# Optimization experiments

Hardware: AMD Instinct MI355X
Metric: run time of the kernel (lower is better)

The kernel has to match this reference:

```python
import jax, jax.numpy as jnp
import numpy as np

EMBED_DIM = 1024
NUM_HEADS = 16
HEAD_DIM = EMBED_DIM // NUM_HEADS


def setup_inputs() -> dict:
    key = jax.random.key(0)
    k_x, k_qkv, k_out = jax.random.split(key, 3)
    x = jax.random.normal(k_x, (4, 2048, EMBED_DIM), dtype=jnp.float32)
    # torch Linear weight [out, in]; y = x @ W.T
    scale = 1.0 / np.sqrt(EMBED_DIM)
    W_qkv = jax.random.uniform(k_qkv, (3 * EMBED_DIM, EMBED_DIM), dtype=jnp.float32, minval=-scale, maxval=scale)
    W_out = jax.random.uniform(k_out, (EMBED_DIM, EMBED_DIM), dtype=jnp.float32, minval=-scale, maxval=scale)
    return {"x": x, "W_qkv": W_qkv, "W_out": W_out}


def reference(x, W_qkv, W_out):
    B, S, E = x.shape
    qkv = jnp.einsum('bse,fe->bsf', x, W_qkv)                     # [B,S,3E]
    qkv = qkv.reshape(B, S, 3, NUM_HEADS, HEAD_DIM)
    qkv = jnp.transpose(qkv, (2, 0, 3, 1, 4))                     # [3,B,H,S,D]
    q, k, v = qkv[0], qkv[1], qkv[2]
    scores = jnp.einsum('bhqd,bhkd->bhqk', q, k) / np.sqrt(HEAD_DIM)
    attn = jax.nn.softmax(scores, axis=-1)                        # dropout_p=0 (eval)
    out = jnp.einsum('bhqk,bhkd->bhqd', attn, v)                  # [B,H,S,D]
    out = jnp.transpose(out, (0, 2, 1, 3)).reshape(B, S, E)
    return jnp.einsum('bse,fe->bsf', out, W_out)
```

## Files before the change

kernel.cpp:

```cpp
#include <hip/hip_runtime.h>
#include <hip/hip_bf16.h>
#include <stdint.h>

#define DEVI __device__ __forceinline__

typedef float  f32x4 __attribute__((ext_vector_type(4)));
typedef short  s16x8 __attribute__((ext_vector_type(8)));

DEVI unsigned short bfbits(float f) {
  __hip_bfloat16 h = __float2bfloat16(f);
  return __builtin_bit_cast(unsigned short, h);
}

DEVI void mfma_bf16(f32x4& d, s16x8 a, s16x8 b) {
  asm("v_mfma_f32_16x16x32_bf16 %0, %1, %2, %0" : "+v"(d) : "v"(a), "v"(b));
}

DEVI void gload_lds16(const void* g, void* l) {
  __builtin_amdgcn_global_load_lds(
      (const __attribute__((address_space(1))) void*)g,
      (__attribute__((address_space(3))) void*)l, 16, 0, 0);
}

__global__ void cvtk(const float4* __restrict__ src, ushort4* __restrict__ dst, int n4) {
  int i = blockIdx.x * blockDim.x + threadIdx.x;
  int st = gridDim.x * blockDim.x;
  for (; i < n4; i += st) {
    float4 v = src[i];
    ushort4 o;
    o.x = bfbits(v.x); o.y = bfbits(v.y); o.z = bfbits(v.z); o.w = bfbits(v.w);
    dst[i] = o;
  }
}

template<int EPI>
__global__ __launch_bounds__(256) void gemm_k(
    const unsigned short* __restrict__ A,
    const unsigned short* __restrict__ BT,
    unsigned short* __restrict__ q_ws,
    unsigned short* __restrict__ k_ws,
    unsigned short* __restrict__ vt_ws,
    float* __restrict__ Cout)
{
  constexpr int K = 1024;
  __shared__ __align__(16) unsigned short Als[128 * 64];
  __shared__ __align__(16) unsigned short Bls[128 * 64];

  const int tid = threadIdx.x;
  const int w = tid >> 6, l = tid & 63;
  const int g = l >> 4, c = l & 15;
  const int wm = w >> 1, wn = w & 1;
  const int nb = blockIdx.x, mb = blockIdx.y;

  int srow[4], skof[4];
#pragma unroll
  for (int it = 0; it < 4; ++it) {
    int idx = (w * 4 + it) * 64 + l;
    srow[it] = idx >> 3;
    skof[it] = ((idx & 7) ^ (srow[it] & 7)) << 3;
  }

  f32x4 acc[4][4] = {};
  const unsigned short* Ab = A + (size_t)(mb * 128) * K;
  const unsigned short* Bb = BT + (size_t)(nb * 128) * K;

  for (int kt = 0; kt < K / 64; ++kt) {
    __syncthreads();
#pragma unroll
    for (int it = 0; it < 4; ++it) {
      gload_lds16(Ab + (size_t)srow[it] * K + kt * 64 + skof[it], &Als[(w * 4 + it) * 512]);
      gload_lds16(Bb + (size_t)srow[it] * K + kt * 64 + skof[it], &Bls[(w * 4 + it) * 512]);
    }
    __syncthreads();
#pragma unroll
    for (int kk = 0; kk < 2; ++kk) {
      s16x8 af[4], bfv[4];
#pragma unroll
      for (int mi = 0; mi < 4; ++mi) {
        int row = wm * 64 + mi * 16 + c;
        int slot = (kk * 4 + g) ^ (row & 7);
        af[mi] = *(const s16x8*)&Als[row * 64 + slot * 8];
      }
#pragma unroll
      for (int ni = 0; ni < 4; ++ni) {
        int row = wn * 64 + ni * 16 + c;
        int slot = (kk * 4 + g) ^ (row & 7);
        bfv[ni] = *(const s16x8*)&Bls[row * 64 + slot * 8];
      }
#pragma unroll
      for (int mi = 0; mi < 4; ++mi)
#pragma unroll
        for (int ni = 0; ni < 4; ++ni)
          mfma_bf16(acc[mi][ni], af[mi], bfv[ni]);
    }
  }

  if constexpr (EPI == 0) {
    const int csec = (nb * 128) >> 10;
#pragma unroll
    for (int mi = 0; mi < 4; ++mi) {
#pragma unroll
      for (int ni = 0; ni < 4; ++ni) {
        int ncol = nb * 128 + wn * 64 + ni * 16 + c;
        int f = ncol & 1023;
        int hh = f >> 6, dd = f & 63;
#pragma unroll
        for (int r = 0; r < 4; ++r) {
          int m = mb * 128 + wm * 64 + mi * 16 + 4 * g + r;
          int bb = m >> 11, ss = m & 2047;
          int bh = bb * 16 + hh;
          float v = acc[mi][ni][r];
          if (csec == 0)      q_ws[((size_t)bh * 2048 + ss) * 64 + dd] = bfbits(v * 0.125f);
          else if (csec == 1) k_ws[((size_t)bh * 2048 + ss) * 64 + dd] = bfbits(v);
          else                vt_ws[((size_t)bh * 64 + dd) * 2048 + ss] = bfbits(v);
        }
      }
    }
  } else {
#pragma unroll
    for (int mi = 0; mi < 4; ++mi)
#pragma unroll
      for (int ni = 0; ni < 4; ++ni) {
        int ncol = nb * 128 + wn * 64 + ni * 16 + c;
#pragma unroll
        for (int r = 0; r < 4; ++r) {
          int m = mb * 128 + wm * 64 + mi * 16 + 4 * g + r;
          Cout[(size_t)m * 1024 + ncol] = acc[mi][ni][r];
        }
      }
  }
}

__global__ __launch_bounds__(256) void attn_k(
    const unsigned short* __restrict__ q_ws,
    const unsigned short* __restrict__ k_ws,
    const unsigned short* __restrict__ vt_ws,
    unsigned short* __restrict__ a_ws)
{
  __shared__ __align__(16) unsigned short P[4][64][40];
  const int tid = threadIdx.x;
  const int w = tid >> 6, l = tid & 63;
  const int g = l >> 4, c = l & 15;
  const int wid = blockIdx.x * 4 + w;
  const int bh = wid >> 5, qt = wid & 31;
  const int b = bh >> 4, h = bh & 15;
  const int qbase = qt * 64;

  const unsigned short* qp = q_ws + (size_t)bh * 2048 * 64;
  const unsigned short* kp = k_ws + (size_t)bh * 2048 * 64;
  const unsigned short* vp = vt_ws + (size_t)bh * 64 * 2048;

  s16x8 qa[4][2];
#pragma unroll
  for (int mi = 0; mi < 4; ++mi)
#pragma unroll
    for (int kk = 0; kk < 2; ++kk)
      qa[mi][kk] = *(const s16x8*)&qp[(size_t)(qbase + mi * 16 + c) * 64 + kk * 32 + g * 8];

  f32x4 o[4][4] = {};
  float lrun[4];
#pragma unroll
  for (int mi = 0; mi < 4; ++mi) lrun[mi] = 0.f;

  s16x8 kb[2][2], vb[4];
#pragma unroll
  for (int nt = 0; nt < 2; ++nt)
#pragma unroll
    for (int kk = 0; kk < 2; ++kk)
      kb[nt][kk] = *(const s16x8*)&kp[(size_t)(nt * 16 + c) * 64 + kk * 32 + g * 8];
#pragma unroll
  for (int dt = 0; dt < 4; ++dt)
    vb[dt] = *(const s16x8*)&vp[(size_t)(dt * 16 + c) * 2048 + g * 8];

  for (int kv = 0; kv < 2048; kv += 32) {
    const int nkv = (kv + 32 < 2048) ? kv + 32 : kv;
    s16x8 kbn[2][2], vbn[4];
#pragma unroll
    for (int nt = 0; nt < 2; ++nt)
#pragma unroll
      for (int kk = 0; kk < 2; ++kk)
        kbn[nt][kk] = *(const s16x8*)&kp[(size_t)(nkv + nt * 16 + c) * 64 + kk * 32 + g * 8];
#pragma unroll
    for (int dt = 0; dt < 4; ++dt)
      vbn[dt] = *(const s16x8*)&vp[(size_t)(dt * 16 + c) * 2048 + nkv + g * 8];

    f32x4 st[4][2] = {};
#pragma unroll
    for (int kk = 0; kk < 2; ++kk)
#pragma unroll
      for (int mi = 0; mi < 4; ++mi)
#pragma unroll
        for (int nt = 0; nt < 2; ++nt)
          mfma_bf16(st[mi][nt], kb[nt][kk], qa[mi][kk]);

#pragma unroll
    for (int mi = 0; mi < 4; ++mi) {
      f32x4 s0 = st[mi][0], s1 = st[mi][1];
      ushort4 w0, w1;
      float p00 = __expf(s0[0]), p01 = __expf(s0[1]);
      float p02 = __expf(s0[2]), p03 = __expf(s0[3]);
      float p10 = __expf(s1[0]), p11 = __expf(s1[1]);
      float p12 = __expf(s1[2]), p13 = __expf(s1[3]);
      lrun[mi] += ((p00 + p01) + (p02 + p03)) + ((p10 + p11) + (p12 + p13));
      w0.x = bfbits(p00); w0.y = bfbits(p01); w0.z = bfbits(p02); w0.w = bfbits(p03);
      w1.x = bfbits(p10); w1.y = bfbits(p11); w1.z = bfbits(p12); w1.w = bfbits(p13);
      *(ushort4*)&P[w][mi * 16 + c][4 * g]      = w0;
      *(ushort4*)&P[w][mi * 16 + c][16 + 4 * g] = w1;
    }

    asm volatile("s_waitcnt lgkmcnt(0)" ::: "memory");
    __builtin_amdgcn_sched_barrier(0);

    s16x8 pa[4];
#pragma unroll
    for (int mi = 0; mi < 4; ++mi)
      pa[mi] = *(const s16x8*)&P[w][mi * 16 + c][g * 8];

    __builtin_amdgcn_sched_barrier(0);
    asm volatile("" ::: "memory");

#pragma unroll
    for (int dt = 0; dt < 4; ++dt)
#pragma unroll
      for (int mi = 0; mi < 4; ++mi)
        mfma_bf16(o[dt][mi], vb[dt], pa[mi]);

#pragma unroll
    for (int nt = 0; nt < 2; ++nt)
#pragma unroll
      for (int kk = 0; kk < 2; ++kk)
        kb[nt][kk] = kbn[nt][kk];
#pragma unroll
    for (int dt = 0; dt < 4; ++dt)
      vb[dt] = vbn[dt];
  }

#pragma unroll
  for (int mi = 0; mi < 4; ++mi) {
    float lv = lrun[mi];
    lv += __shfl_xor(lv, 16);
    lv += __shfl_xor(lv, 32);
    float inv = 1.0f / lv;
    size_t base = ((size_t)(b * 2048 + qbase + mi * 16 + c)) * 1024 + h * 64;
#pragma unroll
    for (int dt = 0; dt < 4; ++dt) {
      ushort4 ov;
      ov.x = bfbits(o[dt][mi][0] * inv);
      ov.y = bfbits(o[dt][mi][1] * inv);
      ov.z = bfbits(o[dt][mi][2] * inv);
      ov.w = bfbits(o[dt][mi][3] * inv);
      *(ushort4*)&a_ws[base + dt * 16 + 4 * g] = ov;
    }
  }
}

extern "C" void kernel_launch(void* const* d_in, const int* in_sizes, int n_in,
                              void* d_out, int out_size, void* d_ws, size_t ws_size,
                              hipStream_t stream) {
  const float* x    = (const float*)d_in[0];
  const float* Wqkv = (const float*)d_in[1];
  const float* Wout = (const float*)d_in[2];

  unsigned short* xb    = (unsigned short*)d_ws;
  unsigned short* wqkvb = xb    + (size_t)8192 * 1024;
  unsigned short* woutb = wqkvb + (size_t)3072 * 1024;
  unsigned short* q_ws  = woutb + (size_t)1024 * 1024;
  unsigned short* k_ws  = q_ws  + (size_t)64 * 2048 * 64;
  unsigned short* vt_ws = k_ws  + (size_t)64 * 2048 * 64;
  unsigned short* a_ws  = xb;

  cvtk<<<1024, 256, 0, stream>>>((const float4*)x,    (ushort4*)xb,    8192 * 1024 / 4);
  cvtk<<<512,  256, 0, stream>>>((const float4*)Wqkv, (ushort4*)wqkvb, 3072 * 1024 / 4);
  cvtk<<<256,  256, 0, stream>>>((const float4*)Wout, (ushort4*)woutb, 1024 * 1024 / 4);

  gemm_k<0><<<dim3(24, 64), 256, 0, stream>>>(xb, wqkvb, q_ws, k_ws, vt_ws, nullptr);
  attn_k<<<512, 256, 0, stream>>>(q_ws, k_ws, vt_ws, a_ws);
  gemm_k<1><<<dim3(8, 64), 256, 0, stream>>>(a_ws, woutb, nullptr, nullptr, nullptr, (float*)d_out);
}
```

Measured before the change: 250.9 us.

## Split attention KV range in two and merge partial outputs

The attention kernel is templated so each query tile processes only half of the key/value sequence. This doubles the grid from 512 to 1024 blocks to fill more of the GPU. Each half writes an unnormalized bf16 partial output and its row sums, and a new merge kernel adds the halves and normalizes. The cost is an extra kernel launch, extra workspace traffic for the partials, and an extra bf16 rounding of the partial outputs. The split path only runs when the workspace is large enough; otherwise the original single-pass path is used.

```diff
diff --git a/kernel.cpp b/kernel.cpp
--- a/kernel.cpp
+++ b/kernel.cpp
@@ -10,6 +10,10 @@
 DEVI unsigned short bfbits(float f) {
   __hip_bfloat16 h = __float2bfloat16(f);
   return __builtin_bit_cast(unsigned short, h);
+}
+DEVI float b2f(unsigned short u) {
+  unsigned int x = ((unsigned int)u) << 16;
+  return __builtin_bit_cast(float, x);
 }
 
 DEVI void mfma_bf16(f32x4& d, s16x8 a, s16x8 b) {
@@ -131,24 +135,32 @@
   }
 }
 
+template<int SPLIT>
 __global__ __launch_bounds__(256) void attn_k(
     const unsigned short* __restrict__ q_ws,
     const unsigned short* __restrict__ k_ws,
     const unsigned short* __restrict__ vt_ws,
-    unsigned short* __restrict__ a_ws)
+    unsigned short* __restrict__ a_ws,
+    unsigned short* __restrict__ opA,
+    unsigned short* __restrict__ opB,
+    float* __restrict__ lA,
+    float* __restrict__ lB)
 {
   __shared__ __align__(16) unsigned short P[4][64][40];
   const int tid = threadIdx.x;
   const int w = tid >> 6, l = tid & 63;
   const int g = l >> 4, c = l & 15;
-  const int wid = blockIdx.x * 4 + w;
+  const int kvh  = SPLIT ? (blockIdx.x >> 9) : 0;
+  const int bidq = SPLIT ? (blockIdx.x & 511) : blockIdx.x;
+  const int wid = bidq * 4 + w;
   const int bh = wid >> 5, qt = wid & 31;
   const int b = bh >> 4, h = bh & 15;
   const int qbase = qt * 64;
+  const int KVLEN = SPLIT ? 1024 : 2048;
 
   const unsigned short* qp = q_ws + (size_t)bh * 2048 * 64;
-  const unsigned short* kp = k_ws + (size_t)bh * 2048 * 64;
-  const unsigned short* vp = vt_ws + (size_t)bh * 64 * 2048;
+  const unsigned short* kp = k_ws + (size_t)bh * 2048 * 64 + (size_t)(kvh * 1024) * 64;
+  const unsigned short* vp = vt_ws + (size_t)bh * 64 * 2048 + (size_t)(kvh * 1024);
 
   s16x8 qa[4][2];
 #pragma unroll
@@ -172,8 +184,8 @@
   for (int dt = 0; dt < 4; ++dt)
     vb[dt] = *(const s16x8*)&vp[(size_t)(dt * 16 + c) * 2048 + g * 8];
 
-  for (int kv = 0; kv < 2048; kv += 32) {
-    const int nkv = (kv + 32 < 2048) ? kv + 32 : kv;
+  for (int kv = 0; kv < KVLEN; kv += 32) {
+    const int nkv = (kv + 32 < KVLEN) ? kv + 32 : kv;
     s16x8 kbn[2][2], vbn[4];
 #pragma unroll
     for (int nt = 0; nt < 2; ++nt)
@@ -235,23 +247,74 @@
       vb[dt] = vbn[dt];
   }
 
-#pragma unroll
-  for (int mi = 0; mi < 4; ++mi) {
-    float lv = lrun[mi];
-    lv += __shfl_xor(lv, 16);
-    lv += __shfl_xor(lv, 32);
-    float inv = 1.0f / lv;
-    size_t base = ((size_t)(b * 2048 + qbase + mi * 16 + c)) * 1024 + h * 64;
-#pragma unroll
-    for (int dt = 0; dt < 4; ++dt) {
-      ushort4 ov;
-      ov.x = bfbits(o[dt][mi][0] * inv);
-      ov.y = bfbits(o[dt][mi][1] * inv);
-      ov.z = bfbits(o[dt][mi][2] * inv);
-      ov.w = bfbits(o[dt][mi][3] * inv);
-      *(ushort4*)&a_ws[base + dt * 16 + 4 * g] = ov;
-    }
-  }
+  if constexpr (SPLIT == 0) {
+#pragma unroll
+    for (int mi = 0; mi < 4; ++mi) {
+      float lv = lrun[mi];
+      lv += __shfl_xor(lv, 16);
+      lv += __shfl_xor(lv, 32);
+      float inv = 1.0f / lv;
+      size_t base = ((size_t)(b * 2048 + qbase + mi * 16 + c)) * 1024 + h * 64;
+#pragma unroll
+      for (int dt = 0; dt < 4; ++dt) {
+        ushort4 ov;
+        ov.x = bfbits(o[dt][mi][0] * inv);
+        ov.y = bfbits(o[dt][mi][1] * inv);
+        ov.z = bfbits(o[dt][mi][2] * inv);
+        ov.w = bfbits(o[dt][mi][3] * inv);
+        *(ushort4*)&a_ws[base + dt * 16 + 4 * g] = ov;
+      }
+    }
+  } else {
+    unsigned short* op = kvh ? opB : opA;
+    float* lp = kvh ? lB : lA;
+#pragma unroll
+    for (int mi = 0; mi < 4; ++mi) {
+      float lv = lrun[mi];
+      lv += __shfl_xor(lv, 16);
+      lv += __shfl_xor(lv, 32);
+      int srow = qbase + mi * 16 + c;
+      if (g == 0) lp[bh * 2048 + srow] = lv;
+      size_t base = ((size_t)(b * 2048 + srow)) * 1024 + h * 64;
+#pragma unroll
+      for (int dt = 0; dt < 4; ++dt) {
+        ushort4 ov;
+        ov.x = bfbits(o[dt][mi][0]);
+        ov.y = bfbits(o[dt][mi][1]);
+        ov.z = bfbits(o[dt][mi][2]);
+        ov.w = bfbits(o[dt][mi][3]);
+        *(ushort4*)&op[base + dt * 16 + 4 * g] = ov;
+      }
+    }
+  }
+}
+
+__global__ __launch_bounds__(256) void mergek(
+    unsigned short* __restrict__ opA,
+    const unsigned short* __restrict__ opB,
+    const float* __restrict__ lA,
+    const float* __restrict__ lB)
+{
+  int i = blockIdx.x * 256 + threadIdx.x;
+  int col = (i & 127) * 8;
+  int rowf = i >> 7;
+  int bb = rowf >> 11, ss = rowf & 2047;
+  int hh = col >> 6;
+  float linv = 1.0f / (lA[(bb * 16 + hh) * 2048 + ss] + lB[(bb * 16 + hh) * 2048 + ss]);
+  size_t off = (size_t)rowf * 1024 + col;
+  ushort4 a0 = *(ushort4*)&opA[off], a1 = *(ushort4*)&opA[off + 4];
+  ushort4 b0 = *(const ushort4*)&opB[off], b1 = *(const ushort4*)&opB[off + 4];
+  ushort4 r0, r1;
+  r0.x = bfbits((b2f(a0.x) + b2f(b0.x)) * linv);
+  r0.y = bfbits((b2f(a0.y) + b2f(b0.y)) * linv);
+  r0.z = bfbits((b2f(a0.z) + b2f(b0.z)) * linv);
+  r0.w = bfbits((b2f(a0.w) + b2f(b0.w)) * linv);
+  r1.x = bfbits((b2f(a1.x) + b2f(b1.x)) * linv);
+  r1.y = bfbits((b2f(a1.y) + b2f(b1.y)) * linv);
+  r1.z = bfbits((b2f(a1.z) + b2f(b1.z)) * linv);
+  r1.w = bfbits((b2f(a1.w) + b2f(b1.w)) * linv);
+  *(ushort4*)&opA[off]     = r0;
+  *(ushort4*)&opA[off + 4] = r1;
 }
 
 extern "C" void kernel_launch(void* const* d_in, const int* in_sizes, int n_in,
@@ -267,13 +330,25 @@
   unsigned short* q_ws  = woutb + (size_t)1024 * 1024;
   unsigned short* k_ws  = q_ws  + (size_t)64 * 2048 * 64;
   unsigned short* vt_ws = k_ws  + (size_t)64 * 2048 * 64;
+  unsigned short* opB   = vt_ws + (size_t)64 * 2048 * 64;
   unsigned short* a_ws  = xb;
+  float* lA = (float*)wqkvb;
+  float* lB = lA + 131072;
+
+  const size_t NEED = ((size_t)8388608 + 3145728 + 1048576 + 3 * 8388608 + 8388608) * 2;
 
   cvtk<<<1024, 256, 0, stream>>>((const float4*)x,    (ushort4*)xb,    8192 * 1024 / 4);
   cvtk<<<512,  256, 0, stream>>>((const float4*)Wqkv, (ushort4*)wqkvb, 3072 * 1024 / 4);
   cvtk<<<256,  256, 0, stream>>>((const float4*)Wout, (ushort4*)woutb, 1024 * 1024 / 4);
 
   gemm_k<0><<<dim3(24, 64), 256, 0, stream>>>(xb, wqkvb, q_ws, k_ws, vt_ws, nullptr);
-  attn_k<<<512, 256, 0, stream>>>(q_ws, k_ws, vt_ws, a_ws);
+
+  if (ws_size >= NEED) {
+    attn_k<1><<<1024, 256, 0, stream>>>(q_ws, k_ws, vt_ws, nullptr, a_ws, opB, lA, lB);
+    mergek<<<4096, 256, 0, stream>>>(a_ws, opB, lA, lB);
+  } else {
+    attn_k<0><<<512, 256, 0, stream>>>(q_ws, k_ws, vt_ws, a_ws, nullptr, nullptr, nullptr, nullptr);
+  }
+
   gemm_k<1><<<dim3(8, 64), 256, 0, stream>>>(a_ws, woutb, nullptr, nullptr, nullptr, (float*)d_out);
 }
```

Measured after the change: 266.4 us. 6.2% more time.

## Stage shared K/V tiles in LDS via direct global-to-LDS loads

Applied to the files above, without the earlier changes.

Each of the four waves in a block previously loaded the same K and V tiles straight from global memory into registers, with register double buffering. The new code has the block cooperatively load each 32-key K/V tile once into XOR-swizzled LDS using global_load_lds, then each wave reads its fragments from LDS. This cuts redundant global and L2 traffic by sharing tiles across the four waves. In exchange it adds two block-wide barriers per iteration and drops the prefetch overlap, so load latency is exposed.

```diff
diff --git a/kernel.cpp b/kernel.cpp
--- a/kernel.cpp
+++ b/kernel.cpp
@@ -137,6 +137,8 @@
     const unsigned short* __restrict__ vt_ws,
     unsigned short* __restrict__ a_ws)
 {
+  __shared__ __align__(16) unsigned short Klds[32 * 64];
+  __shared__ __align__(16) unsigned short Vlds[64 * 32];
   __shared__ __align__(16) unsigned short P[4][64][40];
   const int tid = threadIdx.x;
   const int w = tid >> 6, l = tid & 63;
@@ -150,6 +152,11 @@
   const unsigned short* kp = k_ws + (size_t)bh * 2048 * 64;
   const unsigned short* vp = vt_ws + (size_t)bh * 64 * 2048;
 
+  const int krow  = 8 * w + (l >> 3);
+  const int kslot = (l & 7) ^ (l >> 3);
+  const int vrow  = 16 * w + (l >> 2);
+  const int vslot = (l & 3) ^ ((l >> 3) & 3);
+
   s16x8 qa[4][2];
 #pragma unroll
   for (int mi = 0; mi < 4; ++mi)
@@ -162,27 +169,20 @@
 #pragma unroll
   for (int mi = 0; mi < 4; ++mi) lrun[mi] = 0.f;
 
-  s16x8 kb[2][2], vb[4];
-#pragma unroll
-  for (int nt = 0; nt < 2; ++nt)
-#pragma unroll
-    for (int kk = 0; kk < 2; ++kk)
-      kb[nt][kk] = *(const s16x8*)&kp[(size_t)(nt * 16 + c) * 64 + kk * 32 + g * 8];
-#pragma unroll
-  for (int dt = 0; dt < 4; ++dt)
-    vb[dt] = *(const s16x8*)&vp[(size_t)(dt * 16 + c) * 2048 + g * 8];
-
   for (int kv = 0; kv < 2048; kv += 32) {
-    const int nkv = (kv + 32 < 2048) ? kv + 32 : kv;
-    s16x8 kbn[2][2], vbn[4];
+    __syncthreads();
+    gload_lds16(kp + (size_t)(kv + krow) * 64 + kslot * 8, &Klds[w * 512]);
+    gload_lds16(vp + (size_t)vrow * 2048 + kv + vslot * 8, &Vlds[w * 512]);
+    __syncthreads();
+
+    s16x8 kb[2][2];
 #pragma unroll
     for (int nt = 0; nt < 2; ++nt)
 #pragma unroll
-      for (int kk = 0; kk < 2; ++kk)
-        kbn[nt][kk] = *(const s16x8*)&kp[(size_t)(nkv + nt * 16 + c) * 64 + kk * 32 + g * 8];
-#pragma unroll
-    for (int dt = 0; dt < 4; ++dt)
-      vbn[dt] = *(const s16x8*)&vp[(size_t)(dt * 16 + c) * 2048 + nkv + g * 8];
+      for (int kk = 0; kk < 2; ++kk) {
+        int row = nt * 16 + c;
+        kb[nt][kk] = *(const s16x8*)&Klds[row * 64 + (((kk * 4 + g) ^ (row & 7)) * 8)];
+      }
 
     f32x4 st[4][2] = {};
 #pragma unroll
@@ -211,7 +211,7 @@
     asm volatile("s_waitcnt lgkmcnt(0)" ::: "memory");
     __builtin_amdgcn_sched_barrier(0);
 
-    s16x8 pa[4];
+    s16x8 pa[4], vb[4];
 #pragma unroll
     for (int mi = 0; mi < 4; ++mi)
       pa[mi] = *(const s16x8*)&P[w][mi * 16 + c][g * 8];
@@ -220,19 +220,15 @@
     asm volatile("" ::: "memory");
 
 #pragma unroll
+    for (int dt = 0; dt < 4; ++dt) {
+      int rd = dt * 16 + c;
+      vb[dt] = *(const s16x8*)&Vlds[rd * 32 + ((g ^ ((rd >> 1) & 3)) * 8)];
+    }
+#pragma unroll
     for (int dt = 0; dt < 4; ++dt)
 #pragma unroll
       for (int mi = 0; mi < 4; ++mi)
         mfma_bf16(o[dt][mi], vb[dt], pa[mi]);
-
-#pragma unroll
-    for (int nt = 0; nt < 2; ++nt)
-#pragma unroll
-      for (int kk = 0; kk < 2; ++kk)
-        kb[nt][kk] = kbn[nt][kk];
-#pragma unroll
-    for (int dt = 0; dt < 4; ++dt)
-      vb[dt] = vbn[dt];
   }
 
 #pragma unroll
```

Measured after the change: 220.6 us. 1.14x faster.
